# Performance work log

Measured on AMD Instinct MI355X. Metric: run time of the kernel, lower is better.

## Reference

```python
import jax, jax.numpy as jnp
import numpy as np
import math

DIM = 256
B, S = 4, 2048


def setup_inputs() -> dict:
    key = jax.random.key(0)
    ks = jax.random.split(key, 8)
    h = DIM // 2
    return {
        "features": jax.random.normal(ks[0], (B, S, DIM), dtype=jnp.float32),
        "W1": jax.random.normal(ks[1], (DIM, h), dtype=jnp.float32) / np.sqrt(DIM),
        "b1": jnp.zeros((h,), dtype=jnp.float32),
        "ln_g": jnp.ones((h,), dtype=jnp.float32),
        "ln_b": jnp.zeros((h,), dtype=jnp.float32),
        "W2": jax.random.normal(ks[2], (h, 1), dtype=jnp.float32) / np.sqrt(h),
        "b2": jnp.zeros((1,), dtype=jnp.float32),
        "target_entropy": jnp.full((1,), math.log(DIM), dtype=jnp.float32),
        "temperature": jnp.ones((1,), dtype=jnp.float32),
    }


def _compute_entropy(features, temperature):
    b, s, d = features.shape
    x = features.reshape(-1, d)  # [N, D]
    sq = jnp.sum(x * x, axis=-1)  # [N]
    # squared euclidean distance (cdist(...)**2), clamped for numerical safety
    d2 = jnp.maximum(sq[:, None] + sq[None, :] - 2.0 * (x @ x.T), 0.0)  # [N, N]
    kernel = jnp.exp(-d2 / (2.0 * temperature[0] ** 2))
    probs = kernel / jnp.sum(kernel, axis=-1, keepdims=True)
    entropy = -jnp.sum(probs * jnp.log(probs + 1e-6), axis=-1)
    return entropy.reshape(b, s)


def _entropy_estimator(features, W1, b1, ln_g, ln_b, W2, b2):
    h = features @ W1 + b1  # [B, S, D/2]
    mu = jnp.mean(h, axis=-1, keepdims=True)
    var = jnp.mean((h - mu) ** 2, axis=-1, keepdims=True)
    hn = (h - mu) / jnp.sqrt(var + 1e-5) * ln_g + ln_b
    hg = jax.nn.gelu(hn, approximate=False)
    return (hg @ W2 + b2).squeeze(-1)  # [B, S]


def reference(features, W1, b1, ln_g, ln_b, W2, b2, target_entropy, temperature):
    current_entropy = _compute_entropy(features, temperature)  # [B, S]
    # estimated_entropy is computed in the original forward but unused in outputs
    _est = _entropy_estimator(features, W1, b1, ln_g, ln_b, W2, b2)
    entropy_diff = current_entropy - target_entropy[0]
    control_signal = jax.nn.sigmoid(-entropy_diff / temperature[0])  # [B, S]
    controlled_features = features * control_signal[..., None]
    return controlled_features, control_signal
```

## Files before the change

kernel.cpp:

```cpp
#include <hip/hip_runtime.h>

#define N 8192
#define D 256

typedef short short8 __attribute__((ext_vector_type(8)));
typedef float f32x4 __attribute__((ext_vector_type(4)));

__device__ __forceinline__ unsigned short f2bf(float f) {
    unsigned int u = __float_as_uint(f);
    u += 0x7fffu + ((u >> 16) & 1u);
    return (unsigned short)(u >> 16);
}
__device__ __forceinline__ float bf2f(unsigned short h) {
    return __uint_as_float(((unsigned int)h) << 16);
}

#define GLDS16(g, l) __builtin_amdgcn_global_load_lds(                      \
    (const __attribute__((address_space(1))) void*)(g),                     \
    (__attribute__((address_space(3))) void*)(l), 16, 0, 0)

__global__ __launch_bounds__(64) void k_cvt(const float* __restrict__ x,
                                            unsigned short* __restrict__ xb2,
                                            float* __restrict__ sq,
                                            float* __restrict__ Sarr,
                                            float* __restrict__ Larr) {
    const int lane = threadIdx.x & 63;
    const int c = lane & 15, q8 = lane >> 4;
    const int grp = blockIdx.x;
    const int row = grp * 16 + c;

    float ssum = 0.0f;
#pragma unroll
    for (int kk = 0; kk < 8; ++kk) {
        const float4* gp = (const float4*)(x + (size_t)row * D + kk * 32 + q8 * 8);
        float4 v0 = gp[0], v1 = gp[1];
        unsigned short h[8];
        h[0] = f2bf(v0.x); h[1] = f2bf(v0.y); h[2] = f2bf(v0.z); h[3] = f2bf(v0.w);
        h[4] = f2bf(v1.x); h[5] = f2bf(v1.y); h[6] = f2bf(v1.z); h[7] = f2bf(v1.w);
        short8 p;
#pragma unroll
        for (int i = 0; i < 8; ++i) {
            float f = bf2f(h[i]);
            ssum = fmaf(f, f, ssum);
            p[i] = (short)h[i];
        }
        ((short8*)xb2)[(grp * 8 + kk) * 64 + lane] = p;
    }
    ssum += __shfl_xor(ssum, 16, 64);
    ssum += __shfl_xor(ssum, 32, 64);
    if (q8 == 0) {
        sq[row] = ssum;
        Sarr[row] = 0.0f;
        Larr[row] = 0.0f;
    }
}

__global__ __launch_bounds__(256, 2) void k_gram(const unsigned short* __restrict__ xb2,
                                                 const float* __restrict__ sq,
                                                 const float* __restrict__ temp,
                                                 float* __restrict__ Sarr,
                                                 float* __restrict__ Larr) {
    __shared__ unsigned short Bs[2][64 * D];

    const int tid = threadIdx.x;
    const int wv = tid >> 6, lane = tid & 63;
    const int q8 = lane >> 4, c = lane & 15;
    const int rowbase = blockIdx.x * 256;
    const int ybase = blockIdx.y * 512;
    const float T = temp[0];
    const float LOG2E = 1.44269504f;
    const float s2 = -LOG2E / (2.0f * T * T);
    const float c2 = -2.0f * s2;

    short8 av[4][8];
#pragma unroll
    for (int tr = 0; tr < 4; ++tr) {
        const int grp = (rowbase >> 4) + wv * 4 + tr;
#pragma unroll
        for (int kk = 0; kk < 8; ++kk)
            av[tr][kk] = ((const short8*)xb2)[(grp * 8 + kk) * 64 + lane];
    }
    float ar[16];
#pragma unroll
    for (int tr = 0; tr < 4; ++tr)
#pragma unroll
        for (int r = 0; r < 4; ++r)
            ar[tr * 4 + r] = sq[rowbase + wv * 64 + tr * 16 + q8 * 4 + r] * s2;
    float armax = ar[0];
#pragma unroll
    for (int k = 1; k < 16; ++k) armax = fmaxf(armax, ar[k]);

    float Sr[16], Mr[16];
#pragma unroll
    for (int k = 0; k < 16; ++k) { Sr[k] = 0.f; Mr[k] = 0.f; }

#pragma unroll
    for (int g2 = 0; g2 < 8; ++g2) {
        int s = wv * 8 + g2;
        const unsigned short* src =
            xb2 + (size_t)(ybase >> 4) * 4096 + s * 512 + lane * 8;
        GLDS16(src, &Bs[0][0] + s * 512);
    }

    for (int ht = 0; ht < 8; ++ht) {
        const int tilebase = ybase + ht * 64;
        const int cur = ht & 1;

        __syncthreads();

        if (ht < 7) {
            const size_t nchunk = (size_t)((tilebase + 64) >> 4) * 4096;
#pragma unroll
            for (int g2 = 0; g2 < 8; ++g2) {
                int s = wv * 8 + g2;
                const unsigned short* src = xb2 + nchunk + s * 512 + lane * 8;
                GLDS16(src, &Bs[cur ^ 1][0] + s * 512);
            }
        }

#pragma unroll
        for (int tc = 0; tc < 4; ++tc) {
            const float bc = sq[tilebase + tc * 16 + c] * s2;
            const unsigned short* bb = &Bs[cur][0] + tc * 8 * 512 + lane * 8;

            short8 bva[4];
#pragma unroll
            for (int kk = 0; kk < 4; ++kk)
                bva[kk] = *(const short8*)(bb + kk * 512);

            f32x4 acc[4];
#pragma unroll
            for (int tr = 0; tr < 4; ++tr)
#pragma unroll
                for (int r = 0; r < 4; ++r) acc[tr][r] = 0.0f;

#pragma unroll
            for (int kk = 0; kk < 4; ++kk)
#pragma unroll
                for (int tr = 0; tr < 4; ++tr)
                    acc[tr] = __builtin_amdgcn_mfma_f32_16x16x32_bf16(
                        av[tr][kk], bva[kk], acc[tr], 0, 0, 0);

            short8 bvb[4];
#pragma unroll
            for (int kk = 0; kk < 4; ++kk)
                bvb[kk] = *(const short8*)(bb + (kk + 4) * 512);

#pragma unroll
            for (int kk = 0; kk < 4; ++kk)
#pragma unroll
                for (int tr = 0; tr < 4; ++tr)
                    acc[tr] = __builtin_amdgcn_mfma_f32_16x16x32_bf16(
                        av[tr][kk + 4], bvb[kk], acc[tr], 0, 0, 0);

            float gmax = acc[0][0];
#pragma unroll
            for (int tr = 0; tr < 4; ++tr)
#pragma unroll
                for (int r = 0; r < 4; ++r) gmax = fmaxf(gmax, acc[tr][r]);
            const float bound = fmaf(gmax, c2, armax + bc);

            if (__any(bound >= -115.0f)) {
#pragma unroll
                for (int tr = 0; tr < 4; ++tr)
#pragma unroll
                    for (int r = 0; r < 4; ++r) {
                        float g = acc[tr][r];
                        float t2 = fminf(fmaf(g, c2, ar[tr * 4 + r] + bc), 0.0f);
                        float e = __builtin_amdgcn_exp2f(t2);
                        Sr[tr * 4 + r] += e;
                        Mr[tr * 4 + r] = fmaf(e, t2, Mr[tr * 4 + r]);
                    }
            }
        }
    }

#pragma unroll
    for (int m = 1; m <= 8; m <<= 1)
#pragma unroll
        for (int k = 0; k < 16; ++k) {
            Sr[k] += __shfl_xor(Sr[k], m, 64);
            Mr[k] += __shfl_xor(Mr[k], m, 64);
        }
    if (c == 0) {
        const float LN2 = 0.69314718f;
#pragma unroll
        for (int k = 0; k < 16; ++k) {
            int row = rowbase + wv * 64 + (k >> 2) * 16 + q8 * 4 + (k & 3);
            atomicAdd(&Sarr[row], Sr[k]);
            atomicAdd(&Larr[row], Mr[k] * LN2);
        }
    }
}

__global__ __launch_bounds__(256) void k_finish(const float* __restrict__ x,
                                                const float* __restrict__ Sarr,
                                                const float* __restrict__ Larr,
                                                const float* __restrict__ target,
                                                const float* __restrict__ temp,
                                                float* __restrict__ out) {
    const int gid = blockIdx.x * 256 + threadIdx.x;
    const int row = gid >> 6;
    float S = Sarr[row], L = Larr[row];
    float H = __logf(S) - L / S;
    float z = (H - target[0]) / temp[0];
    float cs = 1.0f / (1.0f + __expf(z));
    float4 v = ((const float4*)x)[gid];
    float4 o;
    o.x = v.x * cs; o.y = v.y * cs; o.z = v.z * cs; o.w = v.w * cs;
    ((float4*)out)[gid] = o;
    if ((gid & 63) == 0) out[(size_t)N * D + row] = cs;
}

extern "C" void kernel_launch(void* const* d_in, const int* in_sizes, int n_in,
                              void* d_out, int out_size, void* d_ws, size_t ws_size,
                              hipStream_t stream) {
    const float* x = (const float*)d_in[0];
    const float* target = (const float*)d_in[7];
    const float* temp = (const float*)d_in[8];
    float* out = (float*)d_out;

    float* wsf = (float*)d_ws;
    float* sq = wsf;
    float* Sarr = wsf + N;
    float* Larr = wsf + 2 * N;

    const size_t need = 3 * (size_t)N * sizeof(float) + (size_t)N * D * sizeof(unsigned short);
    unsigned short* xb2 = (ws_size >= need) ? (unsigned short*)(wsf + 3 * N)
                                            : (unsigned short*)d_out;

    k_cvt<<<N / 16, 64, 0, stream>>>(x, xb2, sq, Sarr, Larr);
    k_gram<<<dim3(32, 16), 256, 0, stream>>>(xb2, sq, temp, Sarr, Larr);
    k_finish<<<(N * (D / 4)) / 256, 256, 0, stream>>>(x, Sarr, Larr, target, temp, out);
}
```

Baseline: 113.6 us.

## Interleave LDS prefetch with MFMA phases using fine-grained barriers and setprio

Splits each 64-column tile of the gram kernel into eight phases. Each phase reads its B fragment from LDS and issues one slice of the next tile's global-to-LDS prefetch. The phases are separated by workgroup barriers, and the MFMA block is raised to high priority with s_setprio. The goal is to stagger waves so that matrix work overlaps with memory and exp work, and to spread the prefetch traffic instead of issuing it all at once. The cost is many more barriers per tile, which can serialize waves and add stall overhead.

Result: faster. 111.2 us (-2.1%).

```diff
diff --git a/kernel.cpp b/kernel.cpp
--- a/kernel.cpp
+++ b/kernel.cpp
@@ -105,73 +105,82 @@
     for (int ht = 0; ht < 8; ++ht) {
         const int tilebase = ybase + ht * 64;
         const int cur = ht & 1;
-
-        __syncthreads();
-
-        if (ht < 7) {
-            const size_t nchunk = (size_t)((tilebase + 64) >> 4) * 4096;
-#pragma unroll
-            for (int g2 = 0; g2 < 8; ++g2) {
-                int s = wv * 8 + g2;
+        const size_t nchunk = (size_t)((tilebase + 64) >> 4) * 4096;
+
+        asm volatile("s_waitcnt vmcnt(0)" ::: "memory");
+        __builtin_amdgcn_sched_barrier(0);
+        __builtin_amdgcn_s_barrier();
+        __builtin_amdgcn_sched_barrier(0);
+
+        float bcv[4];
+#pragma unroll
+        for (int tc = 0; tc < 4; ++tc)
+            bcv[tc] = sq[tilebase + tc * 16 + c] * s2;
+
+        f32x4 acc[4];
+
+#pragma unroll
+        for (int p = 0; p < 8; ++p) {
+            const int tc = p >> 1, half = p & 1;
+            const unsigned short* bb = &Bs[cur][0] + tc * 8 * 512 + lane * 8;
+
+            short8 bv[4];
+#pragma unroll
+            for (int kk = 0; kk < 4; ++kk)
+                bv[kk] = *(const short8*)(bb + (half * 4 + kk) * 512);
+
+            if (ht < 7) {
+                int s = wv * 8 + p;
                 const unsigned short* src = xb2 + nchunk + s * 512 + lane * 8;
                 GLDS16(src, &Bs[cur ^ 1][0] + s * 512);
             }
-        }
-
-#pragma unroll
-        for (int tc = 0; tc < 4; ++tc) {
-            const float bc = sq[tilebase + tc * 16 + c] * s2;
-            const unsigned short* bb = &Bs[cur][0] + tc * 8 * 512 + lane * 8;
-
-            short8 bva[4];
-#pragma unroll
-            for (int kk = 0; kk < 4; ++kk)
-                bva[kk] = *(const short8*)(bb + kk * 512);
-
-            f32x4 acc[4];
-#pragma unroll
-            for (int tr = 0; tr < 4; ++tr)
-#pragma unroll
-                for (int r = 0; r < 4; ++r) acc[tr][r] = 0.0f;
-
+
+            __builtin_amdgcn_sched_barrier(0);
+            __builtin_amdgcn_s_barrier();
+            __builtin_amdgcn_sched_barrier(0);
+
+            if (half == 0) {
+#pragma unroll
+                for (int tr = 0; tr < 4; ++tr)
+#pragma unroll
+                    for (int r = 0; r < 4; ++r) acc[tr][r] = 0.0f;
+            }
+
+            __builtin_amdgcn_s_setprio(1);
 #pragma unroll
             for (int kk = 0; kk < 4; ++kk)
 #pragma unroll
                 for (int tr = 0; tr < 4; ++tr)
                     acc[tr] = __builtin_amdgcn_mfma_f32_16x16x32_bf16(
-                        av[tr][kk], bva[kk], acc[tr], 0, 0, 0);
-
-            short8 bvb[4];
-#pragma unroll
-            for (int kk = 0; kk < 4; ++kk)
-                bvb[kk] = *(const short8*)(bb + (kk + 4) * 512);
-
-#pragma unroll
-            for (int kk = 0; kk < 4; ++kk)
+                        av[tr][half * 4 + kk], bv[kk], acc[tr], 0, 0, 0);
+            __builtin_amdgcn_s_setprio(0);
+            __builtin_amdgcn_sched_barrier(0);
+
+            if (half == 1) {
+                const float bc = bcv[tc];
+                float gmax = acc[0][0];
 #pragma unroll
                 for (int tr = 0; tr < 4; ++tr)
-                    acc[tr] = __builtin_amdgcn_mfma_f32_16x16x32_bf16(
-                        av[tr][kk + 4], bvb[kk], acc[tr], 0, 0, 0);
-
-            float gmax = acc[0][0];
-#pragma unroll
-            for (int tr = 0; tr < 4; ++tr)
-#pragma unroll
-                for (int r = 0; r < 4; ++r) gmax = fmaxf(gmax, acc[tr][r]);
-            const float bound = fmaf(gmax, c2, armax + bc);
-
-            if (__any(bound >= -115.0f)) {
-#pragma unroll
-                for (int tr = 0; tr < 4; ++tr)
-#pragma unroll
-                    for (int r = 0; r < 4; ++r) {
-                        float g = acc[tr][r];
-                        float t2 = fminf(fmaf(g, c2, ar[tr * 4 + r] + bc), 0.0f);
-                        float e = __builtin_amdgcn_exp2f(t2);
-                        Sr[tr * 4 + r] += e;
-                        Mr[tr * 4 + r] = fmaf(e, t2, Mr[tr * 4 + r]);
-                    }
+#pragma unroll
+                    for (int r = 0; r < 4; ++r) gmax = fmaxf(gmax, acc[tr][r]);
+                const float bound = fmaf(gmax, c2, armax + bc);
+
+                if (__any(bound >= -115.0f)) {
+#pragma unroll
+                    for (int tr = 0; tr < 4; ++tr)
+#pragma unroll
+                        for (int r = 0; r < 4; ++r) {
+                            float g = acc[tr][r];
+                            float t2 = fminf(fmaf(g, c2, ar[tr * 4 + r] + bc), 0.0f);
+                            float e = __builtin_amdgcn_exp2f(t2);
+                            Sr[tr * 4 + r] += e;
+                            Mr[tr * 4 + r] = fmaf(e, t2, Mr[tr * 4 + r]);
+                        }
+                }
             }
+
+            __builtin_amdgcn_sched_barrier(0);
+            __builtin_amdgcn_s_barrier();
         }
     }
 
```

## Load Gram B-tiles directly from global into registers instead of LDS double buffer

Applied to the files above, without the earlier changes.

Removes the shared-memory double-buffered staging of column tiles (global_load_lds plus __syncthreads) and instead has each wave load its 16-column B fragments straight from global memory into registers for each of 32 column tiles. This drops the block-wide barriers and the 64KB LDS footprint, which could allow more resident blocks. In exchange each of the 4 waves loads the same B data separately, relying on L1/L2 to serve it, and load latency is no longer explicitly overlapped with compute.

Result: slower. 123.3 us (+8.5%).

```diff
diff --git a/kernel.cpp b/kernel.cpp
--- a/kernel.cpp
+++ b/kernel.cpp
@@ -14,10 +14,6 @@
 __device__ __forceinline__ float bf2f(unsigned short h) {
     return __uint_as_float(((unsigned int)h) << 16);
 }
-
-#define GLDS16(g, l) __builtin_amdgcn_global_load_lds(                      \
-    (const __attribute__((address_space(1))) void*)(g),                     \
-    (__attribute__((address_space(3))) void*)(l), 16, 0, 0)
 
 __global__ __launch_bounds__(64) void k_cvt(const float* __restrict__ x,
                                             unsigned short* __restrict__ xb2,
@@ -60,8 +56,6 @@
                                                  const float* __restrict__ temp,
                                                  float* __restrict__ Sarr,
                                                  float* __restrict__ Larr) {
-    __shared__ unsigned short Bs[2][64 * D];
-
     const int tid = threadIdx.x;
     const int wv = tid >> 6, lane = tid & 63;
     const int q8 = lane >> 4, c = lane & 15;
@@ -94,84 +88,49 @@
 #pragma unroll
     for (int k = 0; k < 16; ++k) { Sr[k] = 0.f; Mr[k] = 0.f; }
 
+    for (int ct = 0; ct < 32; ++ct) {
+        const int colbase = ybase + ct * 16;
+        const int grp = colbase >> 4;
+        const short8* bp = (const short8*)xb2 + (size_t)grp * 8 * 64;
+
+        short8 bv[8];
 #pragma unroll
-    for (int g2 = 0; g2 < 8; ++g2) {
-        int s = wv * 8 + g2;
-        const unsigned short* src =
-            xb2 + (size_t)(ybase >> 4) * 4096 + s * 512 + lane * 8;
-        GLDS16(src, &Bs[0][0] + s * 512);
-    }
+        for (int kk = 0; kk < 8; ++kk)
+            bv[kk] = bp[kk * 64 + lane];
 
-    for (int ht = 0; ht < 8; ++ht) {
-        const int tilebase = ybase + ht * 64;
-        const int cur = ht & 1;
+        const float bc = sq[colbase + c] * s2;
 
-        __syncthreads();
-
-        if (ht < 7) {
-            const size_t nchunk = (size_t)((tilebase + 64) >> 4) * 4096;
+        f32x4 acc[4];
 #pragma unroll
-            for (int g2 = 0; g2 < 8; ++g2) {
-                int s = wv * 8 + g2;
-                const unsigned short* src = xb2 + nchunk + s * 512 + lane * 8;
-                GLDS16(src, &Bs[cur ^ 1][0] + s * 512);
-            }
-        }
+        for (int tr = 0; tr < 4; ++tr)
+#pragma unroll
+            for (int r = 0; r < 4; ++r) acc[tr][r] = 0.0f;
 
 #pragma unroll
-        for (int tc = 0; tc < 4; ++tc) {
-            const float bc = sq[tilebase + tc * 16 + c] * s2;
-            const unsigned short* bb = &Bs[cur][0] + tc * 8 * 512 + lane * 8;
+        for (int kk = 0; kk < 8; ++kk)
+#pragma unroll
+            for (int tr = 0; tr < 4; ++tr)
+                acc[tr] = __builtin_amdgcn_mfma_f32_16x16x32_bf16(
+                    av[tr][kk], bv[kk], acc[tr], 0, 0, 0);
 
-            short8 bva[4];
+        float gmax = acc[0][0];
 #pragma unroll
-            for (int kk = 0; kk < 4; ++kk)
-                bva[kk] = *(const short8*)(bb + kk * 512);
+        for (int tr = 0; tr < 4; ++tr)
+#pragma unroll
+            for (int r = 0; r < 4; ++r) gmax = fmaxf(gmax, acc[tr][r]);
+        const float bound = fmaf(gmax, c2, armax + bc);
 
-            f32x4 acc[4];
+        if (__any(bound >= -115.0f)) {
 #pragma unroll
             for (int tr = 0; tr < 4; ++tr)
 #pragma unroll
-                for (int r = 0; r < 4; ++r) acc[tr][r] = 0.0f;
-
-#pragma unroll
-            for (int kk = 0; kk < 4; ++kk)
-#pragma unroll
-                for (int tr = 0; tr < 4; ++tr)
-                    acc[tr] = __builtin_amdgcn_mfma_f32_16x16x32_bf16(
-                        av[tr][kk], bva[kk], acc[tr], 0, 0, 0);
-
-            short8 bvb[4];
-#pragma unroll
-            for (int kk = 0; kk < 4; ++kk)
-                bvb[kk] = *(const short8*)(bb + (kk + 4) * 512);
-
-#pragma unroll
-            for (int kk = 0; kk < 4; ++kk)
-#pragma unroll
-                for (int tr = 0; tr < 4; ++tr)
-                    acc[tr] = __builtin_amdgcn_mfma_f32_16x16x32_bf16(
-                        av[tr][kk + 4], bvb[kk], acc[tr], 0, 0, 0);
-
-            float gmax = acc[0][0];
-#pragma unroll
-            for (int tr = 0; tr < 4; ++tr)
-#pragma unroll
-                for (int r = 0; r < 4; ++r) gmax = fmaxf(gmax, acc[tr][r]);
-            const float bound = fmaf(gmax, c2, armax + bc);
-
-            if (__any(bound >= -115.0f)) {
-#pragma unroll
-                for (int tr = 0; tr < 4; ++tr)
-#pragma unroll
-                    for (int r = 0; r < 4; ++r) {
-                        float g = acc[tr][r];
-                        float t2 = fminf(fmaf(g, c2, ar[tr * 4 + r] + bc), 0.0f);
-                        float e = __builtin_amdgcn_exp2f(t2);
-                        Sr[tr * 4 + r] += e;
-                        Mr[tr * 4 + r] = fmaf(e, t2, Mr[tr * 4 + r]);
-                    }
-            }
+                for (int r = 0; r < 4; ++r) {
+                    float g = acc[tr][r];
+                    float t2 = fminf(fmaf(g, c2, ar[tr * 4 + r] + bc), 0.0f);
+                    float e = __builtin_amdgcn_exp2f(t2);
+                    Sr[tr * 4 + r] += e;
+                    Mr[tr * 4 + r] = fmaf(e, t2, Mr[tr * 4 + r]);
+                }
         }
     }
 
```
